# Kernel optimization log

Hardware: AMD Instinct MI355X
Metric: run time of the kernel (lower is better)

The kernel has to match this reference:

```python
import jax, jax.numpy as jnp
import numpy as np
import math

B, L, DIM, DEPTH, HEADS, DH, T, BUCKETS, MAXDIST = 256, 77, 768, 12, 12, 64, 1000, 32, 128
INNER = HEADS * DH            # 768
FF_IN = 4 * DIM               # 3072 (SwiGLU inner)
EPS = 1e-5


def rmsnorm(x, gamma):
    inv = jax.lax.rsqrt(jnp.sum(x * x, axis=-1, keepdims=True) + EPS)
    return x * inv * gamma * (DIM ** 0.5)


def rel_pos_bias(i, j, table):
    # table: [BUCKETS, HEADS] -> bias [HEADS, i, j]
    q_pos = jnp.arange(i)
    k_pos = jnp.arange(j)
    rel = k_pos[None, :] - q_pos[:, None]
    n = jnp.maximum(-rel, 0)
    max_exact = BUCKETS // 2
    is_small = n < max_exact
    nf = jnp.maximum(n, 1).astype(jnp.float32)
    val_large = max_exact + (jnp.log(nf / max_exact) / math.log(MAXDIST / max_exact) * (BUCKETS - max_exact)).astype(jnp.int32)
    val_large = jnp.minimum(val_large, BUCKETS - 1)
    bucket = jnp.where(is_small, n, val_large)
    return jnp.transpose(table[bucket], (2, 0, 1))  # h i j


def attention(x, mask, bias, gamma, Wq, Wkv, Wout, null_kv):
    b, n, _ = x.shape
    xn = rmsnorm(x, gamma)
    q = (xn @ Wq).reshape(b, n, HEADS, DH).transpose(0, 2, 1, 3)     # b h n d
    kv = xn @ Wkv                                                     # b n 2d (single head)
    k, v = kv[..., :DH], kv[..., DH:]
    nk = jnp.broadcast_to(null_kv[0], (b, 1, DH))
    nv = jnp.broadcast_to(null_kv[1], (b, 1, DH))
    k = jnp.concatenate([nk, k], axis=1)                              # b (n+1) d
    v = jnp.concatenate([nv, v], axis=1)
    sim = jnp.einsum('bhid,bjd->bhij', q * (DH ** -0.5), k) + bias[None]
    neg = -jnp.finfo(sim.dtype).max
    m = jnp.pad(mask, ((0, 0), (1, 0)), constant_values=True)         # null kv always visible
    sim = jnp.where(m[:, None, None, :], sim, neg)
    i, j = n, n + 1
    causal = jnp.arange(j)[None, :] > (jnp.arange(i)[:, None] + (j - i))
    sim = jnp.where(causal[None, None], neg, sim)
    attn = jax.nn.softmax(sim - jax.lax.stop_gradient(sim.max(axis=-1, keepdims=True)), axis=-1)
    out = jnp.einsum('bhij,bjd->bhid', attn, v)
    out = out.transpose(0, 2, 1, 3).reshape(b, n, INNER)
    return out @ Wout


def feedforward(x, gamma, W1, W2):
    h = rmsnorm(x, gamma) @ W1                                        # b n 2*FF_IN
    a, gate = h[..., :FF_IN], h[..., FF_IN:]
    return (a * jax.nn.silu(gate)) @ W2


def setup_inputs() -> dict:
    key = jax.random.key(0)
    ks = jax.random.split(key, 16)
    s = 0.02
    return {
        'image_embed': jax.random.normal(ks[0], (B, DIM), jnp.float32),
        'text_encodings': jax.random.normal(ks[1], (B, L, DIM), jnp.float32),
        'text_embed': jax.random.normal(ks[2], (B, DIM), jnp.float32),
        'time_emb_table': jax.random.normal(ks[3], (T, DIM), jnp.float32) * s,
        'learned_query': jax.random.normal(ks[4], (DIM,), jnp.float32),
        'rel_bias_table': jax.random.normal(ks[5], (BUCKETS, HEADS), jnp.float32) * s,
        'attn_gamma': jnp.ones((DEPTH, DIM), jnp.float32),
        'Wq': jax.random.normal(ks[6], (DEPTH, DIM, INNER), jnp.float32) * s,
        'Wkv': jax.random.normal(ks[7], (DEPTH, DIM, 2 * DH), jnp.float32) * s,
        'Wout': jax.random.normal(ks[8], (DEPTH, INNER, DIM), jnp.float32) * s,
        'null_kv': jax.random.normal(ks[9], (DEPTH, 2, DH), jnp.float32),
        'ff_gamma': jnp.ones((DEPTH, DIM), jnp.float32),
        'Wff1': jax.random.normal(ks[10], (DEPTH, DIM, 2 * FF_IN), jnp.float32) * s,
        'Wff2': jax.random.normal(ks[11], (DEPTH, FF_IN, DIM), jnp.float32) * s,
        'diffusion_timesteps': jax.random.randint(ks[12], (B,), 0, T),
        'mask': jnp.ones((B, L), dtype=bool),
    }


def reference(image_embed, text_encodings, text_embed, time_emb_table, learned_query,
              rel_bias_table, attn_gamma, Wq, Wkv, Wout, null_kv, ff_gamma, Wff1, Wff2,
              diffusion_timesteps, mask):
    b = image_embed.shape[0]
    # mask bookkeeping (matches torch forward); cond_drop_prob fixed at 1.0 -> keep all
    not_all = jnp.any(mask, axis=-1)
    m = jnp.concatenate([mask, not_all[:, None]], axis=1)
    m = jnp.pad(m, ((0, 0), (0, 2)), constant_values=True)            # [b, L+3]
    time_embed = time_emb_table[diffusion_timesteps][:, None, :]
    queries = jnp.broadcast_to(learned_query, (b, 1, DIM))
    tokens = jnp.concatenate([text_encodings, text_embed[:, None, :], time_embed, queries], axis=1)
    n = tokens.shape[1]
    bias = rel_pos_bias(n, n + 1, rel_bias_table)
    x = tokens
    for l in range(DEPTH):
        x = attention(x, m, bias, attn_gamma[l], Wq[l], Wkv[l], Wout[l], null_kv[l]) + x
        x = feedforward(x, ff_gamma[l], Wff1[l], Wff2[l]) + x
    return x[:, -1, :]
```

## Files before the change

### kernel.cpp

```cpp
#include <hip/hip_runtime.h>
#include <hip/hip_bf16.h>
#include <float.h>
#include <math.h>

#define NB 256
#define LTXT 77
#define DIM 768
#define DEPTH 12
#define HEADS 12
#define DH 64
#define NTOK 80
#define NKEY 81
#define NROWS (NB*NTOK)
#define FFH 3072
#define FF2C 6144
#define INNER 768
#define SROW 100

typedef __hip_bfloat16 bf16;
typedef __attribute__((ext_vector_type(8))) short short8;
typedef __attribute__((ext_vector_type(4))) float f32x4;

#define BARRIER() asm volatile("s_barrier" ::: "memory")
#define WAITV(n)  asm volatile("s_waitcnt vmcnt(" #n ")" ::: "memory")

__device__ __forceinline__ unsigned short f2bf(float f) {
    __hip_bfloat16 h = __float2bfloat16(f);
    return __builtin_bit_cast(unsigned short, h);
}

__global__ void build_tokens(const float* __restrict__ text_enc,
                             const float* __restrict__ text_emb,
                             const float* __restrict__ time_tab,
                             const float* __restrict__ lquery,
                             const int* __restrict__ tsteps,
                             float* __restrict__ x) {
    int idx = blockIdx.x * 256 + threadIdx.x;
    if (idx >= NROWS * DIM) return;
    int d = idx % DIM;
    int row = idx / DIM;
    int b = row / NTOK, p = row % NTOK;
    float v;
    if (p < LTXT)            v = text_enc[((size_t)b * LTXT + p) * DIM + d];
    else if (p == LTXT)      v = text_emb[(size_t)b * DIM + d];
    else if (p == LTXT + 1)  v = time_tab[(size_t)tsteps[b] * DIM + d];
    else                     v = lquery[d];
    x[idx] = v;
}

__global__ void build_biasR(const float* __restrict__ table, float* __restrict__ biasR) {
    int idx = blockIdx.x * 256 + threadIdx.x;
    if (idx >= HEADS * NTOK * 96) return;
    int kap = idx % 96;
    int i = (idx / 96) % NTOK;
    int h = idx / (96 * NTOK);
    float v;
    if ((kap < 80 && kap > i) || kap > 80) {
        v = -1e30f;
    } else {
        int j = (kap < 80) ? kap + 1 : 0;
        int rel = j - i;
        int n = rel < 0 ? -rel : 0;
        int bucket;
        if (n < 16) {
            bucket = n;
        } else {
            float val = logf((float)n / 16.0f) / logf(8.0f) * 16.0f;
            int vl = 16 + (int)val;
            bucket = vl < 31 ? vl : 31;
        }
        v = table[bucket * HEADS + h];
    }
    biasR[idx] = v;
}

__global__ __launch_bounds__(256) void convT(const float* __restrict__ W,
                                             bf16* __restrict__ WT,
                                             int K, int N) {
    __shared__ float t[32][33];
    int n0 = blockIdx.x * 32, k0 = blockIdx.y * 32;
    int tx = threadIdx.x & 31, ty = threadIdx.x >> 5;
    #pragma unroll
    for (int i = 0; i < 4; i++)
        t[ty + 8 * i][tx] = W[(size_t)(k0 + ty + 8 * i) * N + n0 + tx];
    __syncthreads();
    #pragma unroll
    for (int i = 0; i < 4; i++)
        WT[(size_t)(n0 + ty + 8 * i) * K + k0 + tx] = __float2bfloat16(t[tx][ty + 8 * i]);
}

__global__ __launch_bounds__(256) void rmsnorm_w(const float* __restrict__ x,
                                                 const float* __restrict__ gamma,
                                                 bf16* __restrict__ out) {
    int wave = blockIdx.x * 4 + (threadIdx.x >> 6);
    int lane = threadIdx.x & 63;
    float4 g0 = *(const float4*)&gamma[lane * 4];
    float4 g1 = *(const float4*)&gamma[lane * 4 + 256];
    float4 g2 = *(const float4*)&gamma[lane * 4 + 512];
    #pragma unroll 2
    for (int rr = 0; rr < 8; ++rr) {
        int row = wave * 8 + rr;
        const float* xr = x + (size_t)row * DIM + lane * 4;
        float4 v0 = *(const float4*)xr;
        float4 v1 = *(const float4*)(xr + 256);
        float4 v2 = *(const float4*)(xr + 512);
        float ss = v0.x*v0.x + v0.y*v0.y + v0.z*v0.z + v0.w*v0.w
                 + v1.x*v1.x + v1.y*v1.y + v1.z*v1.z + v1.w*v1.w
                 + v2.x*v2.x + v2.y*v2.y + v2.z*v2.z + v2.w*v2.w;
        #pragma unroll
        for (int o = 32; o > 0; o >>= 1) ss += __shfl_xor(ss, o);
        float inv = 27.712812921102035f / sqrtf(ss + 1e-5f);
        bf16* orow = out + (size_t)row * DIM + lane * 4;
        ushort4 w0 = { f2bf(v0.x*inv*g0.x), f2bf(v0.y*inv*g0.y), f2bf(v0.z*inv*g0.z), f2bf(v0.w*inv*g0.w) };
        ushort4 w1 = { f2bf(v1.x*inv*g1.x), f2bf(v1.y*inv*g1.y), f2bf(v1.z*inv*g1.z), f2bf(v1.w*inv*g1.w) };
        ushort4 w2 = { f2bf(v2.x*inv*g2.x), f2bf(v2.y*inv*g2.y), f2bf(v2.z*inv*g2.z), f2bf(v2.w*inv*g2.w) };
        *(ushort4*)(orow)       = w0;
        *(ushort4*)(orow + 256) = w1;
        *(ushort4*)(orow + 512) = w2;
    }
}


#define GSTAGE_N(nld, lds, base, b0, ld, kk0)                                  \
    _Pragma("unroll")                                                          \
    for (int r_ = 0; r_ < (nld); ++r_) {                                       \
        int idx_ = r_ * 256 + t;                                               \
        int row_ = idx_ >> 3, c_ = idx_ & 7;                                   \
        int cs_ = c_ ^ (row_ & 7);                                             \
        __builtin_amdgcn_global_load_lds(                                      \
            (const __attribute__((address_space(1))) unsigned int*)            \
                &base[(size_t)(b0 + row_) * ld + (kk0) + cs_ * 8],             \
            (__attribute__((address_space(3))) unsigned int*)&lds[idx_ * 8],   \
            16, 0, 0);                                                         \
    }

#define FRAG_READ(dst, lds, base_row, kk)                                      \
    _Pragma("unroll")                                                          \
    for (int q_ = 0; q_ < 4; ++q_) {                                           \
        int row_ = (base_row) + q_ * 16 + fr;                                  \
        int ch_ = ((((kk) << 2) + kb) ^ (row_ & 7));                           \
        dst[q_] = *(const short8*)&lds[row_ * 64 + ch_ * 8];                   \
    }

#define FRAG_READ2(dst, lds, base_row, kk)                                     \
    _Pragma("unroll")                                                          \
    for (int q_ = 0; q_ < 2; ++q_) {                                           \
        int row_ = (base_row) + q_ * 16 + fr;                                  \
        int ch_ = ((((kk) << 2) + kb) ^ (row_ & 7));                           \
        dst[q_] = *(const short8*)&lds[row_ * 64 + ch_ * 8];                   \
    }

template<int EPI>
__global__ __launch_bounds__(256, 2) void gemm_bt(const bf16* __restrict__ A,
                                                  const bf16* __restrict__ BT,
                                                  float* __restrict__ C,
                                                  int N, int K) {
    __shared__ __align__(16) short As[2 * 128 * 64];
    __shared__ __align__(16) short Bs[2 * 128 * 64];
    const int t = threadIdx.x;
    const int lane = t & 63;
    const int wid = t >> 6;
    const int wr = wid >> 1, wc = wid & 1;
    const int fr = lane & 15;
    const int kb = lane >> 4;
    const int row0 = blockIdx.y * 128, col0 = blockIdx.x * 128;

    f32x4 acc[4][4] = {};
    const int NKT = K >> 6;

    GSTAGE_N(4, As, A, row0, K, 0)
    GSTAGE_N(4, Bs, BT, col0, K, 0)

    for (int kt = 0; kt < NKT; ++kt) {
        const short* curA = As + (kt & 1) * (128 * 64);
        const short* curB = Bs + (kt & 1) * (128 * 64);
        if (kt + 1 < NKT) {
            short* nxtA = As + ((kt + 1) & 1) * (128 * 64);
            short* nxtB = Bs + ((kt + 1) & 1) * (128 * 64);
            int k0n = (kt + 1) << 6;
            GSTAGE_N(4, nxtA, A, row0, K, k0n)
            GSTAGE_N(4, nxtB, BT, col0, K, k0n)
            WAITV(8);
        } else {
            WAITV(0);
        }
        BARRIER();
        #pragma unroll
        for (int kk = 0; kk < 2; ++kk) {
            short8 af[4], bv[4];
            FRAG_READ(af, curA, wr * 64, kk)
            FRAG_READ(bv, curB, wc * 64, kk)
            __builtin_amdgcn_s_setprio(1);
            #pragma unroll
            for (int i = 0; i < 4; ++i)
                #pragma unroll
                for (int j = 0; j < 4; ++j)
                    acc[i][j] = __builtin_amdgcn_mfma_f32_16x16x32_bf16(af[i], bv[j], acc[i][j], 0, 0, 0);
            __builtin_amdgcn_s_setprio(0);
        }
        BARRIER();
    }

    #pragma unroll
    for (int i = 0; i < 4; ++i) {
        #pragma unroll
        for (int j = 0; j < 4; ++j) {
            int row = row0 + wr * 64 + i * 16 + kb * 4;
            int col = col0 + wc * 64 + j * 16 + fr;
            #pragma unroll
            for (int r = 0; r < 4; ++r) {
                size_t o = (size_t)(row + r) * N + col;
                if (EPI == 1)      C[o] += acc[i][j][r];
                else               ((bf16*)C)[o] = __float2bfloat16(acc[i][j][r]);
            }
        }
    }
}

__global__ __launch_bounds__(256, 2) void gemm_kv(const bf16* __restrict__ A,
                                                  const bf16* __restrict__ BT,
                                                  bf16* __restrict__ kout,
                                                  bf16* __restrict__ vT) {
    __shared__ __align__(16) short As[2 * 128 * 64];
    __shared__ __align__(16) short Bs[2 * 128 * 64];
    const int t = threadIdx.x;
    const int lane = t & 63;
    const int wid = t >> 6;
    const int wr = wid >> 1, wc = wid & 1;
    const int fr = lane & 15;
    const int kb = lane >> 4;
    const int row0 = blockIdx.y * 128;
    const int K = DIM;

    f32x4 acc[4][4] = {};
    const int NKT = DIM >> 6;

    GSTAGE_N(4, As, A, row0, K, 0)
    GSTAGE_N(4, Bs, BT, 0, K, 0)

    for (int kt = 0; kt < NKT; ++kt) {
        const short* curA = As + (kt & 1) * (128 * 64);
        const short* curB = Bs + (kt & 1) * (128 * 64);
        if (kt + 1 < NKT) {
            short* nxtA = As + ((kt + 1) & 1) * (128 * 64);
            short* nxtB = Bs + ((kt + 1) & 1) * (128 * 64);
            int k0n = (kt + 1) << 6;
            GSTAGE_N(4, nxtA, A, row0, K, k0n)
            GSTAGE_N(4, nxtB, BT, 0, K, k0n)
            WAITV(8);
        } else {
            WAITV(0);
        }
        BARRIER();
        #pragma unroll
        for (int kk = 0; kk < 2; ++kk) {
            short8 af[4], bv[4];
            FRAG_READ(af, curA, wr * 64, kk)
            FRAG_READ(bv, curB, wc * 64, kk)
            __builtin_amdgcn_s_setprio(1);
            #pragma unroll
            for (int i = 0; i < 4; ++i)
                #pragma unroll
                for (int j = 0; j < 4; ++j)
                    acc[i][j] = __builtin_amdgcn_mfma_f32_16x16x32_bf16(af[i], bv[j], acc[i][j], 0, 0, 0);
            __builtin_amdgcn_s_setprio(0);
        }
        BARRIER();
    }

    #pragma unroll
    for (int i = 0; i < 4; ++i) {
        #pragma unroll
        for (int j = 0; j < 4; ++j) {
            int row = row0 + wr * 64 + i * 16 + kb * 4;
            int col = wc * 64 + j * 16 + fr;
            #pragma unroll
            for (int r = 0; r < 4; ++r) {
                int rg = row + r;
                float v = acc[i][j][r];
                if (wc == 0) {
                    kout[(size_t)rg * 64 + col] = __float2bfloat16(v);
                } else {
                    int bb = rg / NTOK, ii = rg - bb * NTOK;
                    vT[((size_t)bb * 64 + (col - 64)) * NTOK + ii] = __float2bfloat16(v);
                }
            }
        }
    }
}

__global__ __launch_bounds__(256) void attn_mfma(const bf16* __restrict__ qb,
                                                 const bf16* __restrict__ kbuf,
                                                 const bf16* __restrict__ vT,
                                                 const float* __restrict__ nullkv,
                                                 const float* __restrict__ biasR,
                                                 bf16* __restrict__ attnb) {
    const int b = blockIdx.x / HEADS;
    const int h = blockIdx.x % HEADS;
    __shared__ __align__(16) short Ks[96 * 64];
    __shared__ __align__(16) short Vt[64 * 128];
    __shared__ __align__(16) float Sls[80 * SROW];
    char* Sb = (char*)Sls;
    const int t = threadIdx.x;
    const int lane = t & 63;
    const int wid = t >> 6;
    const int g = lane >> 4;
    const int fr = lane & 15;

    for (int c = t; c < 768; c += 256) {
        int row = c >> 3, ch = c & 7;
        short8 v;
        if (row < NTOK) {
            v = *(const short8*)&kbuf[((size_t)(b * NTOK + row)) * 64 + ch * 8];
        } else if (row == NTOK) {
            #pragma unroll
            for (int e = 0; e < 8; ++e) v[e] = (short)f2bf(nullkv[ch * 8 + e]);
        } else {
            v = short8{0,0,0,0,0,0,0,0};
        }
        *(short8*)((char*)Ks + row * 128 + ((ch ^ (row & 7)) << 4)) = v;
    }
    for (int c = t; c < 1024; c += 256) {
        int d = c >> 4, ch = c & 15;
        if (ch >= 12) continue;
        short8 v;
        if (ch < 10) {
            v = *(const short8*)&vT[((size_t)b * 64 + d) * NTOK + ch * 8];
        } else if (ch == 10) {
            v = short8{0,0,0,0,0,0,0,0};
            v[0] = (short)f2bf(nullkv[64 + d]);
        } else {
            v = short8{0,0,0,0,0,0,0,0};
        }
        *(short8*)((char*)Vt + d * 256 + ((ch ^ (d & 7)) << 4)) = v;
    }
    __syncthreads();

    const bf16* qbase = qb + ((size_t)(b * NTOK)) * INNER + h * DH;
    for (int s = 0; s < 8; ++s) {
        int tt = wid + 4 * s;
        if (tt >= 30) break;
        int m = tt / 6, n = tt - 6 * m;
        f32x4 acc = {};
        #pragma unroll
        for (int kk = 0; kk < 2; ++kk) {
            short8 a = *(const short8*)&qbase[(size_t)(m * 16 + fr) * INNER + kk * 32 + g * 8];
            int krow = n * 16 + fr;
            short8 kf = *(const short8*)((const char*)Ks + krow * 128 + ((((kk << 2) + g) ^ (krow & 7)) << 4));
            acc = __builtin_amdgcn_mfma_f32_16x16x32_bf16(a, kf, acc, 0, 0, 0);
        }
        int i0 = m * 16 + g * 4;
        int kap = n * 16 + fr;
        const float* bR = biasR + ((size_t)h * NTOK + i0) * 96 + kap;
        #pragma unroll
        for (int r = 0; r < 4; ++r)
            Sls[(i0 + r) * SROW + kap] = acc[r] * 0.125f + bR[r * 96];
    }
    __syncthreads();

    for (int rr = 0; rr < 20; ++rr) {
        int row = wid + 4 * rr;
        const float* Srow = Sls + row * SROW;
        float s0 = Srow[lane];
        float s1v = Srow[64 + (lane & 31)];
        float mx = fmaxf(s0, s1v);
        #pragma unroll
        for (int o = 32; o > 0; o >>= 1) mx = fmaxf(mx, __shfl_xor(mx, o));
        float e0 = __expf(s0 - mx);
        float e1 = (lane < 32) ? __expf(s1v - mx) : 0.0f;
        float sum = e0 + e1;
        #pragma unroll
        for (int o = 32; o > 0; o >>= 1) sum += __shfl_xor(sum, o);
        float inv = 1.0f / sum;
        *(unsigned short*)(Sb + row * (SROW * 4) + lane * 2) = f2bf(e0 * inv);
        if (lane < 32)
            *(unsigned short*)(Sb + row * (SROW * 4) + 128 + lane * 2) = f2bf(e1 * inv);
    }
    __syncthreads();

    for (int s = 0; s < 5; ++s) {
        int tt = wid + 4 * s;
        int m = tt >> 2, n = tt & 3;
        f32x4 acc = {};
        #pragma unroll
        for (int kc = 0; kc < 3; ++kc) {
            short8 p = *(const short8*)(Sb + (m * 16 + fr) * (SROW * 4) + kc * 64 + g * 16);
            int drow = n * 16 + fr;
            short8 vv = *(const short8*)((const char*)Vt + drow * 256 + ((((kc << 2) + g) ^ (drow & 7)) << 4));
            acc = __builtin_amdgcn_mfma_f32_16x16x32_bf16(p, vv, acc, 0, 0, 0);
        }
        int i0 = m * 16 + g * 4;
        int d = n * 16 + fr;
        #pragma unroll
        for (int r = 0; r < 4; ++r)
            attnb[((size_t)(b * NTOK) + i0 + r) * INNER + h * DH + d] = __float2bfloat16(acc[r]);
    }
}

__global__ __launch_bounds__(256, 2) void gemm_ff1(const bf16* __restrict__ A,
                                                   const bf16* __restrict__ W1T,
                                                   bf16* __restrict__ act) {
    __shared__ __align__(16) short As[2 * 128 * 64];
    __shared__ __align__(16) short Bs1[2 * 64 * 64];
    __shared__ __align__(16) short Bs2[2 * 64 * 64];
    const int t = threadIdx.x;
    const int lane = t & 63;
    const int wid = t >> 6;
    const int wr = wid >> 1, wc = wid & 1;
    const int fr = lane & 15;
    const int kb = lane >> 4;
    const int row0 = blockIdx.y * 128, col0 = blockIdx.x * 64;
    const int K = DIM;
    const bf16* B1 = W1T;
    const bf16* B2 = W1T + (size_t)FFH * DIM;

    f32x4 acc1[4][2] = {}, acc2[4][2] = {};
    const int NKT = DIM >> 6;

    GSTAGE_N(4, As, A, row0, K, 0)
    GSTAGE_N(2, Bs1, B1, col0, K, 0)
    GSTAGE_N(2, Bs2, B2, col0, K, 0)

    for (int kt = 0; kt < NKT; ++kt) {
        const short* curA  = As  + (kt & 1) * (128 * 64);
        const short* curB1 = Bs1 + (kt & 1) * (64 * 64);
        const short* curB2 = Bs2 + (kt & 1) * (64 * 64);
        if (kt + 1 < NKT) {
            short* nxtA  = As  + ((kt + 1) & 1) * (128 * 64);
            short* nxtB1 = Bs1 + ((kt + 1) & 1) * (64 * 64);
            short* nxtB2 = Bs2 + ((kt + 1) & 1) * (64 * 64);
            int k0n = (kt + 1) << 6;
            GSTAGE_N(4, nxtA, A, row0, K, k0n)
            GSTAGE_N(2, nxtB1, B1, col0, K, k0n)
            GSTAGE_N(2, nxtB2, B2, col0, K, k0n)
            WAITV(8);
        } else {
            WAITV(0);
        }
        BARRIER();
        #pragma unroll
        for (int kk = 0; kk < 2; ++kk) {
            short8 af[4], b1v[2], b2v[2];
            FRAG_READ(af, curA, wr * 64, kk)
            FRAG_READ2(b1v, curB1, wc * 32, kk)
            FRAG_READ2(b2v, curB2, wc * 32, kk)
            __builtin_amdgcn_s_setprio(1);
            #pragma unroll
            for (int i = 0; i < 4; ++i)
                #pragma unroll
                for (int j = 0; j < 2; ++j) {
                    acc1[i][j] = __builtin_amdgcn_mfma_f32_16x16x32_bf16(af[i], b1v[j], acc1[i][j], 0, 0, 0);
                    acc2[i][j] = __builtin_amdgcn_mfma_f32_16x16x32_bf16(af[i], b2v[j], acc2[i][j], 0, 0, 0);
                }
            __builtin_amdgcn_s_setprio(0);
        }
        BARRIER();
    }

    #pragma unroll
    for (int i = 0; i < 4; ++i) {
        #pragma unroll
        for (int j = 0; j < 2; ++j) {
            int row = row0 + wr * 64 + i * 16 + kb * 4;
            int col = col0 + wc * 32 + j * 16 + fr;
            #pragma unroll
            for (int r = 0; r < 4; ++r) {
                float a = acc1[i][j][r];
                float gt = acc2[i][j][r];
                float s = a * gt / (1.0f + __expf(-gt));
                act[(size_t)(row + r) * FFH + col] = __float2bfloat16(s);
            }
        }
    }
}

__global__ void extract(const float* __restrict__ x, float* __restrict__ out) {
    int idx = blockIdx.x * 256 + threadIdx.x;
    if (idx >= NB * DIM) return;
    int b = idx / DIM, d = idx % DIM;
    out[idx] = x[((size_t)(b * NTOK + NTOK - 1)) * DIM + d];
}

extern "C" void kernel_launch(void* const* d_in, const int* in_sizes, int n_in,
                              void* d_out, int out_size, void* d_ws, size_t ws_size,
                              hipStream_t stream) {
    (void)in_sizes; (void)n_in; (void)out_size; (void)ws_size;
    const float* text_enc = (const float*)d_in[1];
    const float* text_emb = (const float*)d_in[2];
    const float* time_tab = (const float*)d_in[3];
    const float* lquery   = (const float*)d_in[4];
    const float* rel_tab  = (const float*)d_in[5];
    const float* attn_g   = (const float*)d_in[6];
    const float* Wq       = (const float*)d_in[7];
    const float* Wkv      = (const float*)d_in[8];
    const float* Wout     = (const float*)d_in[9];
    const float* null_kv  = (const float*)d_in[10];
    const float* ff_g     = (const float*)d_in[11];
    const float* Wff1     = (const float*)d_in[12];
    const float* Wff2     = (const float*)d_in[13];
    const int*   tsteps   = (const int*)d_in[14];

    char* ws = (char*)d_ws;
    float* x     = (float*)(ws);
    bf16*  xn    = (bf16*)(ws + 62914560);
    bf16*  attnb = xn;
    char*  U     = ws + 94371840;
    bf16*  qb    = (bf16*)U;
    bf16*  kbuf  = (bf16*)(U + 31457280);
    bf16*  vT    = (bf16*)(U + 34078720);
    bf16*  act   = (bf16*)U;
    float* biasR = (float*)(ws + 220200960);
    bf16*  WqT   = (bf16*)(ws + 220569600);
    bf16*  WkvT  = (bf16*)(ws + 221749248);
    bf16*  WoutT = (bf16*)(ws + 221945856);
    bf16*  Wff1T = (bf16*)(ws + 223125504);
    bf16*  Wff2T = (bf16*)(ws + 232562688);

    build_tokens<<<(NROWS * DIM + 255) / 256, 256, 0, stream>>>(text_enc, text_emb, time_tab, lquery, tsteps, x);
    build_biasR<<<(HEADS * NTOK * 96 + 255) / 256, 256, 0, stream>>>(rel_tab, biasR);

    for (int l = 0; l < DEPTH; l++) {
        convT<<<dim3(INNER / 32, DIM / 32), 256, 0, stream>>>(Wq   + (size_t)l * DIM * INNER,  WqT,   DIM,   INNER);
        convT<<<dim3((2 * DH) / 32, DIM / 32), 256, 0, stream>>>(Wkv + (size_t)l * DIM * 2 * DH, WkvT, DIM, 2 * DH);
        convT<<<dim3(DIM / 32, INNER / 32), 256, 0, stream>>>(Wout + (size_t)l * INNER * DIM,  WoutT, INNER, DIM);
        convT<<<dim3(FF2C / 32, DIM / 32), 256, 0, stream>>>(Wff1 + (size_t)l * DIM * FF2C,    Wff1T, DIM,   FF2C);
        convT<<<dim3(DIM / 32, FFH / 32), 256, 0, stream>>>(Wff2  + (size_t)l * FFH * DIM,     Wff2T, FFH,   DIM);

        rmsnorm_w<<<NROWS / (8 * 4), 256, 0, stream>>>(x, attn_g + (size_t)l * DIM, xn);
        gemm_bt<2><<<dim3(INNER / 128, NROWS / 128), 256, 0, stream>>>(xn, WqT, (float*)qb, INNER, DIM);
        gemm_kv<<<dim3(1, NROWS / 128), 256, 0, stream>>>(xn, WkvT, kbuf, vT);
        attn_mfma<<<NB * HEADS, 256, 0, stream>>>(qb, kbuf, vT, null_kv + (size_t)l * 2 * DH, biasR, attnb);
        gemm_bt<1><<<dim3(DIM / 128, NROWS / 128), 256, 0, stream>>>(attnb, WoutT, x, DIM, INNER);

        rmsnorm_w<<<NROWS / (8 * 4), 256, 0, stream>>>(x, ff_g + (size_t)l * DIM, xn);
        gemm_ff1<<<dim3(FFH / 64, NROWS / 128), 256, 0, stream>>>(xn, Wff1T, act);
        gemm_bt<1><<<dim3(DIM / 128, NROWS / 128), 256, 0, stream>>>(act, Wff2T, x, DIM, FFH);
    }

    extract<<<(NB * DIM + 255) / 256, 256, 0, stream>>>(x, (float*)d_out);
}
```

Measured before the change: 7.894 ms.

## Switch GEMMs to 256x256 tiles with 8 waves and split A-tile prefetch

The 128-tile GEMM kernels are replaced with 256-row tile versions that use 512 threads (8 waves). Each wave computes 128 rows, handled as two halves. The next A tile is prefetched between the two half-compute phases, while the B tile is loaded ahead of them, so global loads overlap with MFMA work. The larger tiles raise data reuse per LDS byte and cut global traffic. In exchange, each block needs more LDS and more accumulator registers, and the N=768 GEMMs launch only 240 blocks, which may leave CUs idle.

```diff
diff --git a/kernel.cpp b/kernel.cpp
--- a/kernel.cpp
+++ b/kernel.cpp
@@ -134,6 +134,19 @@
             16, 0, 0);                                                         \
     }
 
+#define GSTAGE512(nld, lds, base, b0, ld, kk0)                                 \
+    _Pragma("unroll")                                                          \
+    for (int r_ = 0; r_ < (nld); ++r_) {                                       \
+        int idx_ = r_ * 512 + t;                                               \
+        int row_ = idx_ >> 3, c_ = idx_ & 7;                                   \
+        int cs_ = c_ ^ (row_ & 7);                                             \
+        __builtin_amdgcn_global_load_lds(                                      \
+            (const __attribute__((address_space(1))) unsigned int*)            \
+                &base[(size_t)(b0 + row_) * ld + (kk0) + cs_ * 8],             \
+            (__attribute__((address_space(3))) unsigned int*)&lds[idx_ * 8],   \
+            16, 0, 0);                                                         \
+    }
+
 #define FRAG_READ(dst, lds, base_row, kk)                                      \
     _Pragma("unroll")                                                          \
     for (int q_ = 0; q_ < 4; ++q_) {                                           \
@@ -142,76 +155,217 @@
         dst[q_] = *(const short8*)&lds[row_ * 64 + ch_ * 8];                   \
     }
 
-#define FRAG_READ2(dst, lds, base_row, kk)                                     \
-    _Pragma("unroll")                                                          \
-    for (int q_ = 0; q_ < 2; ++q_) {                                           \
-        int row_ = (base_row) + q_ * 16 + fr;                                  \
-        int ch_ = ((((kk) << 2) + kb) ^ (row_ & 7));                           \
-        dst[q_] = *(const short8*)&lds[row_ * 64 + ch_ * 8];                   \
-    }
+#define LDS_FRAG(lds, row_, kk)                                                \
+    (*(const short8*)&(lds)[(row_) * 64 + ((((kk) << 2) + kb) ^ ((row_) & 7)) * 8])
 
 template<int EPI>
-__global__ __launch_bounds__(256, 2) void gemm_bt(const bf16* __restrict__ A,
-                                                  const bf16* __restrict__ BT,
-                                                  float* __restrict__ C,
-                                                  int N, int K) {
-    __shared__ __align__(16) short As[2 * 128 * 64];
-    __shared__ __align__(16) short Bs[2 * 128 * 64];
+__global__ __launch_bounds__(512, 2) void gemm_bt256(const bf16* __restrict__ A,
+                                                     const bf16* __restrict__ BT,
+                                                     float* __restrict__ C,
+                                                     int N, int K) {
+    __shared__ __align__(16) short As[2 * 256 * 64];
+    __shared__ __align__(16) short Bs[2 * 256 * 64];
     const int t = threadIdx.x;
     const int lane = t & 63;
     const int wid = t >> 6;
-    const int wr = wid >> 1, wc = wid & 1;
+    const int wr = wid >> 2;
+    const int wn = wid & 3;
     const int fr = lane & 15;
     const int kb = lane >> 4;
-    const int row0 = blockIdx.y * 128, col0 = blockIdx.x * 128;
-
-    f32x4 acc[4][4] = {};
+    const int row0 = blockIdx.y * 256, col0 = blockIdx.x * 256;
+
+    f32x4 acc[8][4] = {};
     const int NKT = K >> 6;
 
-    GSTAGE_N(4, As, A, row0, K, 0)
-    GSTAGE_N(4, Bs, BT, col0, K, 0)
+    GSTAGE512(4, Bs, BT, col0, K, 0)
+    GSTAGE512(4, As, A, row0, K, 0)
 
     for (int kt = 0; kt < NKT; ++kt) {
-        const short* curA = As + (kt & 1) * (128 * 64);
-        const short* curB = Bs + (kt & 1) * (128 * 64);
+        const short* curA = As + (kt & 1) * (256 * 64);
+        const short* curB = Bs + (kt & 1) * (256 * 64);
+        short* nxtA = As + ((kt + 1) & 1) * (256 * 64);
+        short* nxtB = Bs + ((kt + 1) & 1) * (256 * 64);
+        const int k0n = (kt + 1) << 6;
+
+        short8 bv[4][2];
         if (kt + 1 < NKT) {
-            short* nxtA = As + ((kt + 1) & 1) * (128 * 64);
-            short* nxtB = Bs + ((kt + 1) & 1) * (128 * 64);
-            int k0n = (kt + 1) << 6;
-            GSTAGE_N(4, nxtA, A, row0, K, k0n)
-            GSTAGE_N(4, nxtB, BT, col0, K, k0n)
-            WAITV(8);
+            GSTAGE512(4, nxtB, BT, col0, K, k0n)
+            WAITV(4);
         } else {
             WAITV(0);
         }
         BARRIER();
-        #pragma unroll
-        for (int kk = 0; kk < 2; ++kk) {
-            short8 af[4], bv[4];
-            FRAG_READ(af, curA, wr * 64, kk)
-            FRAG_READ(bv, curB, wc * 64, kk)
+        {
+            #pragma unroll
+            for (int n = 0; n < 4; ++n)
+                #pragma unroll
+                for (int kk = 0; kk < 2; ++kk)
+                    bv[n][kk] = LDS_FRAG(curB, wn * 64 + n * 16 + fr, kk);
+            short8 af[4][2];
+            #pragma unroll
+            for (int m = 0; m < 4; ++m)
+                #pragma unroll
+                for (int kk = 0; kk < 2; ++kk)
+                    af[m][kk] = LDS_FRAG(curA, wr * 128 + m * 16 + fr, kk);
             __builtin_amdgcn_s_setprio(1);
             #pragma unroll
-            for (int i = 0; i < 4; ++i)
-                #pragma unroll
-                for (int j = 0; j < 4; ++j)
-                    acc[i][j] = __builtin_amdgcn_mfma_f32_16x16x32_bf16(af[i], bv[j], acc[i][j], 0, 0, 0);
+            for (int kk = 0; kk < 2; ++kk)
+                #pragma unroll
+                for (int m = 0; m < 4; ++m)
+                    #pragma unroll
+                    for (int n = 0; n < 4; ++n)
+                        acc[m][n] = __builtin_amdgcn_mfma_f32_16x16x32_bf16(af[m][kk], bv[n][kk], acc[m][n], 0, 0, 0);
             __builtin_amdgcn_s_setprio(0);
         }
         BARRIER();
+        if (kt + 1 < NKT) {
+            GSTAGE512(4, nxtA, A, row0, K, k0n)
+        }
+        BARRIER();
+        {
+            short8 af[4][2];
+            #pragma unroll
+            for (int m = 0; m < 4; ++m)
+                #pragma unroll
+                for (int kk = 0; kk < 2; ++kk)
+                    af[m][kk] = LDS_FRAG(curA, wr * 128 + (m + 4) * 16 + fr, kk);
+            __builtin_amdgcn_s_setprio(1);
+            #pragma unroll
+            for (int kk = 0; kk < 2; ++kk)
+                #pragma unroll
+                for (int m = 0; m < 4; ++m)
+                    #pragma unroll
+                    for (int n = 0; n < 4; ++n)
+                        acc[m + 4][n] = __builtin_amdgcn_mfma_f32_16x16x32_bf16(af[m][kk], bv[n][kk], acc[m + 4][n], 0, 0, 0);
+            __builtin_amdgcn_s_setprio(0);
+        }
+        BARRIER();
     }
 
     #pragma unroll
-    for (int i = 0; i < 4; ++i) {
-        #pragma unroll
-        for (int j = 0; j < 4; ++j) {
-            int row = row0 + wr * 64 + i * 16 + kb * 4;
-            int col = col0 + wc * 64 + j * 16 + fr;
+    for (int m = 0; m < 8; ++m) {
+        #pragma unroll
+        for (int n = 0; n < 4; ++n) {
+            int row = row0 + wr * 128 + m * 16 + kb * 4;
+            int col = col0 + wn * 64 + n * 16 + fr;
             #pragma unroll
             for (int r = 0; r < 4; ++r) {
                 size_t o = (size_t)(row + r) * N + col;
-                if (EPI == 1)      C[o] += acc[i][j][r];
-                else               ((bf16*)C)[o] = __float2bfloat16(acc[i][j][r]);
+                if (EPI == 1)      C[o] += acc[m][n][r];
+                else               ((bf16*)C)[o] = __float2bfloat16(acc[m][n][r]);
+            }
+        }
+    }
+}
+
+__global__ __launch_bounds__(512, 2) void gemm_ff1_256(const bf16* __restrict__ A,
+                                                       const bf16* __restrict__ W1T,
+                                                       bf16* __restrict__ act) {
+    __shared__ __align__(16) short As[2 * 256 * 64];
+    __shared__ __align__(16) short Bs1[2 * 128 * 64];
+    __shared__ __align__(16) short Bs2[2 * 128 * 64];
+    const int t = threadIdx.x;
+    const int lane = t & 63;
+    const int wid = t >> 6;
+    const int wr = wid >> 2;
+    const int wn = wid & 3;
+    const int fr = lane & 15;
+    const int kb = lane >> 4;
+    const int row0 = blockIdx.y * 256, col0 = blockIdx.x * 128;
+    const int K = DIM;
+    const bf16* B1 = W1T;
+    const bf16* B2 = W1T + (size_t)FFH * DIM;
+
+    f32x4 acc1[8][2] = {}, acc2[8][2] = {};
+    const int NKT = DIM >> 6;
+
+    GSTAGE512(2, Bs1, B1, col0, K, 0)
+    GSTAGE512(2, Bs2, B2, col0, K, 0)
+    GSTAGE512(4, As, A, row0, K, 0)
+
+    for (int kt = 0; kt < NKT; ++kt) {
+        const short* curA  = As  + (kt & 1) * (256 * 64);
+        const short* curB1 = Bs1 + (kt & 1) * (128 * 64);
+        const short* curB2 = Bs2 + (kt & 1) * (128 * 64);
+        short* nxtA  = As  + ((kt + 1) & 1) * (256 * 64);
+        short* nxtB1 = Bs1 + ((kt + 1) & 1) * (128 * 64);
+        short* nxtB2 = Bs2 + ((kt + 1) & 1) * (128 * 64);
+        const int k0n = (kt + 1) << 6;
+
+        short8 b1v[2][2], b2v[2][2];
+        if (kt + 1 < NKT) {
+            GSTAGE512(2, nxtB1, B1, col0, K, k0n)
+            GSTAGE512(2, nxtB2, B2, col0, K, k0n)
+            WAITV(4);
+        } else {
+            WAITV(0);
+        }
+        BARRIER();
+        {
+            #pragma unroll
+            for (int n = 0; n < 2; ++n)
+                #pragma unroll
+                for (int kk = 0; kk < 2; ++kk) {
+                    b1v[n][kk] = LDS_FRAG(curB1, wn * 32 + n * 16 + fr, kk);
+                    b2v[n][kk] = LDS_FRAG(curB2, wn * 32 + n * 16 + fr, kk);
+                }
+            short8 af[4][2];
+            #pragma unroll
+            for (int m = 0; m < 4; ++m)
+                #pragma unroll
+                for (int kk = 0; kk < 2; ++kk)
+                    af[m][kk] = LDS_FRAG(curA, wr * 128 + m * 16 + fr, kk);
+            __builtin_amdgcn_s_setprio(1);
+            #pragma unroll
+            for (int kk = 0; kk < 2; ++kk)
+                #pragma unroll
+                for (int m = 0; m < 4; ++m)
+                    #pragma unroll
+                    for (int n = 0; n < 2; ++n) {
+                        acc1[m][n] = __builtin_amdgcn_mfma_f32_16x16x32_bf16(af[m][kk], b1v[n][kk], acc1[m][n], 0, 0, 0);
+                        acc2[m][n] = __builtin_amdgcn_mfma_f32_16x16x32_bf16(af[m][kk], b2v[n][kk], acc2[m][n], 0, 0, 0);
+                    }
+            __builtin_amdgcn_s_setprio(0);
+        }
+        BARRIER();
+        if (kt + 1 < NKT) {
+            GSTAGE512(4, nxtA, A, row0, K, k0n)
+        }
+        BARRIER();
+        {
+            short8 af[4][2];
+            #pragma unroll
+            for (int m = 0; m < 4; ++m)
+                #pragma unroll
+                for (int kk = 0; kk < 2; ++kk)
+                    af[m][kk] = LDS_FRAG(curA, wr * 128 + (m + 4) * 16 + fr, kk);
+            __builtin_amdgcn_s_setprio(1);
+            #pragma unroll
+            for (int kk = 0; kk < 2; ++kk)
+                #pragma unroll
+                for (int m = 0; m < 4; ++m)
+                    #pragma unroll
+                    for (int n = 0; n < 2; ++n) {
+                        acc1[m + 4][n] = __builtin_amdgcn_mfma_f32_16x16x32_bf16(af[m][kk], b1v[n][kk], acc1[m + 4][n], 0, 0, 0);
+                        acc2[m + 4][n] = __builtin_amdgcn_mfma_f32_16x16x32_bf16(af[m][kk], b2v[n][kk], acc2[m + 4][n], 0, 0, 0);
+                    }
+            __builtin_amdgcn_s_setprio(0);
+        }
+        BARRIER();
+    }
+
+    #pragma unroll
+    for (int m = 0; m < 8; ++m) {
+        #pragma unroll
+        for (int n = 0; n < 2; ++n) {
+            int row = row0 + wr * 128 + m * 16 + kb * 4;
+            int col = col0 + wn * 32 + n * 16 + fr;
+            #pragma unroll
+            for (int r = 0; r < 4; ++r) {
+                float a = acc1[m][n][r];
+                float gt = acc2[m][n][r];
+                float s = a * gt / (1.0f + __expf(-gt));
+                act[(size_t)(row + r) * FFH + col] = __float2bfloat16(s);
             }
         }
     }
@@ -394,83 +548,6 @@
         #pragma unroll
         for (int r = 0; r < 4; ++r)
             attnb[((size_t)(b * NTOK) + i0 + r) * INNER + h * DH + d] = __float2bfloat16(acc[r]);
-    }
-}
-
-__global__ __launch_bounds__(256, 2) void gemm_ff1(const bf16* __restrict__ A,
-                                                   const bf16* __restrict__ W1T,
-                                                   bf16* __restrict__ act) {
-    __shared__ __align__(16) short As[2 * 128 * 64];
-    __shared__ __align__(16) short Bs1[2 * 64 * 64];
-    __shared__ __align__(16) short Bs2[2 * 64 * 64];
-    const int t = threadIdx.x;
-    const int lane = t & 63;
-    const int wid = t >> 6;
-    const int wr = wid >> 1, wc = wid & 1;
-    const int fr = lane & 15;
-    const int kb = lane >> 4;
-    const int row0 = blockIdx.y * 128, col0 = blockIdx.x * 64;
-    const int K = DIM;
-    const bf16* B1 = W1T;
-    const bf16* B2 = W1T + (size_t)FFH * DIM;
-
-    f32x4 acc1[4][2] = {}, acc2[4][2] = {};
-    const int NKT = DIM >> 6;
-
-    GSTAGE_N(4, As, A, row0, K, 0)
-    GSTAGE_N(2, Bs1, B1, col0, K, 0)
-    GSTAGE_N(2, Bs2, B2, col0, K, 0)
-
-    for (int kt = 0; kt < NKT; ++kt) {
-        const short* curA  = As  + (kt & 1) * (128 * 64);
-        const short* curB1 = Bs1 + (kt & 1) * (64 * 64);
-        const short* curB2 = Bs2 + (kt & 1) * (64 * 64);
-        if (kt + 1 < NKT) {
-            short* nxtA  = As  + ((kt + 1) & 1) * (128 * 64);
-            short* nxtB1 = Bs1 + ((kt + 1) & 1) * (64 * 64);
-            short* nxtB2 = Bs2 + ((kt + 1) & 1) * (64 * 64);
-            int k0n = (kt + 1) << 6;
-            GSTAGE_N(4, nxtA, A, row0, K, k0n)
-            GSTAGE_N(2, nxtB1, B1, col0, K, k0n)
-            GSTAGE_N(2, nxtB2, B2, col0, K, k0n)
-            WAITV(8);
-        } else {
-            WAITV(0);
-        }
-        BARRIER();
-        #pragma unroll
-        for (int kk = 0; kk < 2; ++kk) {
-            short8 af[4], b1v[2], b2v[2];
-            FRAG_READ(af, curA, wr * 64, kk)
-            FRAG_READ2(b1v, curB1, wc * 32, kk)
-            FRAG_READ2(b2v, curB2, wc * 32, kk)
-            __builtin_amdgcn_s_setprio(1);
-            #pragma unroll
-            for (int i = 0; i < 4; ++i)
-                #pragma unroll
-                for (int j = 0; j < 2; ++j) {
-                    acc1[i][j] = __builtin_amdgcn_mfma_f32_16x16x32_bf16(af[i], b1v[j], acc1[i][j], 0, 0, 0);
-                    acc2[i][j] = __builtin_amdgcn_mfma_f32_16x16x32_bf16(af[i], b2v[j], acc2[i][j], 0, 0, 0);
-                }
-            __builtin_amdgcn_s_setprio(0);
-        }
-        BARRIER();
-    }
-
-    #pragma unroll
-    for (int i = 0; i < 4; ++i) {
-        #pragma unroll
-        for (int j = 0; j < 2; ++j) {
-            int row = row0 + wr * 64 + i * 16 + kb * 4;
-            int col = col0 + wc * 32 + j * 16 + fr;
-            #pragma unroll
-            for (int r = 0; r < 4; ++r) {
-                float a = acc1[i][j][r];
-                float gt = acc2[i][j][r];
-                float s = a * gt / (1.0f + __expf(-gt));
-                act[(size_t)(row + r) * FFH + col] = __float2bfloat16(s);
-            }
-        }
     }
 }
 
@@ -527,14 +604,14 @@
         convT<<<dim3(DIM / 32, FFH / 32), 256, 0, stream>>>(Wff2  + (size_t)l * FFH * DIM,     Wff2T, FFH,   DIM);
 
         rmsnorm_w<<<NROWS / (8 * 4), 256, 0, stream>>>(x, attn_g + (size_t)l * DIM, xn);
-        gemm_bt<2><<<dim3(INNER / 128, NROWS / 128), 256, 0, stream>>>(xn, WqT, (float*)qb, INNER, DIM);
+        gemm_bt256<2><<<dim3(INNER / 256, NROWS / 256), 512, 0, stream>>>(xn, WqT, (float*)qb, INNER, DIM);
         gemm_kv<<<dim3(1, NROWS / 128), 256, 0, stream>>>(xn, WkvT, kbuf, vT);
         attn_mfma<<<NB * HEADS, 256, 0, stream>>>(qb, kbuf, vT, null_kv + (size_t)l * 2 * DH, biasR, attnb);
-        gemm_bt<1><<<dim3(DIM / 128, NROWS / 128), 256, 0, stream>>>(attnb, WoutT, x, DIM, INNER);
+        gemm_bt256<1><<<dim3(DIM / 256, NROWS / 256), 512, 0, stream>>>(attnb, WoutT, x, DIM, INNER);
 
         rmsnorm_w<<<NROWS / (8 * 4), 256, 0, stream>>>(x, ff_g + (size_t)l * DIM, xn);
-        gemm_ff1<<<dim3(FFH / 64, NROWS / 128), 256, 0, stream>>>(xn, Wff1T, act);
-        gemm_bt<1><<<dim3(DIM / 128, NROWS / 128), 256, 0, stream>>>(act, Wff2T, x, DIM, FFH);
+        gemm_ff1_256<<<dim3(FFH / 128, NROWS / 256), 512, 0, stream>>>(xn, Wff1T, act);
+        gemm_bt256<1><<<dim3(DIM / 256, NROWS / 256), 512, 0, stream>>>(act, Wff2T, x, DIM, FFH);
     }
 
     extract<<<(NB * DIM + 255) / 256, 256, 0, stream>>>(x, (float*)d_out);
```

Result: no change. 8.004 ms (+1.4%).

## Switch GEMMs to 32x32x16 MFMA and fuse Q and KV projections

Applied to the files above, without the earlier changes.

Replaces the 16x16x32 bf16 MFMA tiles in all GEMM kernels with 32x32x16 MFMA tiles. Each wave now holds 2x2 32x32 accumulators, which roughly halves the LDS fragment reads per unit of work and uses the higher-throughput instruction shape. The Q projection and the KV projection are also merged into one GEMM over a concatenated transposed weight, with a column-dependent epilogue, removing one launch and a second read of the normalized activations. The epilogue stores become strided across rows in a different pattern, which may change write coalescing.

```diff
diff --git a/kernel.cpp b/kernel.cpp
--- a/kernel.cpp
+++ b/kernel.cpp
@@ -20,6 +20,7 @@
 typedef __hip_bfloat16 bf16;
 typedef __attribute__((ext_vector_type(8))) short short8;
 typedef __attribute__((ext_vector_type(4))) float f32x4;
+typedef __attribute__((ext_vector_type(16))) float f32x16;
 
 #define BARRIER() asm volatile("s_barrier" ::: "memory")
 #define WAITV(n)  asm volatile("s_waitcnt vmcnt(" #n ")" ::: "memory")
@@ -134,38 +135,26 @@
             16, 0, 0);                                                         \
     }
 
-#define FRAG_READ(dst, lds, base_row, kk)                                      \
-    _Pragma("unroll")                                                          \
-    for (int q_ = 0; q_ < 4; ++q_) {                                           \
-        int row_ = (base_row) + q_ * 16 + fr;                                  \
-        int ch_ = ((((kk) << 2) + kb) ^ (row_ & 7));                           \
-        dst[q_] = *(const short8*)&lds[row_ * 64 + ch_ * 8];                   \
-    }
-
-#define FRAG_READ2(dst, lds, base_row, kk)                                     \
-    _Pragma("unroll")                                                          \
-    for (int q_ = 0; q_ < 2; ++q_) {                                           \
-        int row_ = (base_row) + q_ * 16 + fr;                                  \
-        int ch_ = ((((kk) << 2) + kb) ^ (row_ & 7));                           \
-        dst[q_] = *(const short8*)&lds[row_ * 64 + ch_ * 8];                   \
-    }
+#define FRAG32(lds, base_row, mm, kk)                                          \
+    (*(const short8*)&(lds)[((base_row) + (mm) * 32 + fr32) * 64 +             \
+        ((((kk) * 2 + hk) ^ (((base_row) + (mm) * 32 + fr32) & 7)) * 8)])
 
 template<int EPI>
-__global__ __launch_bounds__(256, 2) void gemm_bt(const bf16* __restrict__ A,
-                                                  const bf16* __restrict__ BT,
-                                                  float* __restrict__ C,
-                                                  int N, int K) {
+__global__ __launch_bounds__(256, 2) void gemm_bt32(const bf16* __restrict__ A,
+                                                    const bf16* __restrict__ BT,
+                                                    float* __restrict__ C,
+                                                    int N, int K) {
     __shared__ __align__(16) short As[2 * 128 * 64];
     __shared__ __align__(16) short Bs[2 * 128 * 64];
     const int t = threadIdx.x;
     const int lane = t & 63;
     const int wid = t >> 6;
     const int wr = wid >> 1, wc = wid & 1;
-    const int fr = lane & 15;
-    const int kb = lane >> 4;
+    const int fr32 = lane & 31;
+    const int hk = lane >> 5;
     const int row0 = blockIdx.y * 128, col0 = blockIdx.x * 128;
 
-    f32x4 acc[4][4] = {};
+    f32x16 acc[2][2] = {};
     const int NKT = K >> 6;
 
     GSTAGE_N(4, As, A, row0, K, 0)
@@ -185,58 +174,69 @@
             WAITV(0);
         }
         BARRIER();
-        #pragma unroll
-        for (int kk = 0; kk < 2; ++kk) {
-            short8 af[4], bv[4];
-            FRAG_READ(af, curA, wr * 64, kk)
-            FRAG_READ(bv, curB, wc * 64, kk)
+        {
+            short8 af[2][4], bv[2][4];
+            #pragma unroll
+            for (int m = 0; m < 2; ++m)
+                #pragma unroll
+                for (int kk = 0; kk < 4; ++kk)
+                    af[m][kk] = FRAG32(curA, wr * 64, m, kk);
+            #pragma unroll
+            for (int n = 0; n < 2; ++n)
+                #pragma unroll
+                for (int kk = 0; kk < 4; ++kk)
+                    bv[n][kk] = FRAG32(curB, wc * 64, n, kk);
             __builtin_amdgcn_s_setprio(1);
             #pragma unroll
-            for (int i = 0; i < 4; ++i)
-                #pragma unroll
-                for (int j = 0; j < 4; ++j)
-                    acc[i][j] = __builtin_amdgcn_mfma_f32_16x16x32_bf16(af[i], bv[j], acc[i][j], 0, 0, 0);
+            for (int kk = 0; kk < 4; ++kk)
+                #pragma unroll
+                for (int m = 0; m < 2; ++m)
+                    #pragma unroll
+                    for (int n = 0; n < 2; ++n)
+                        acc[m][n] = __builtin_amdgcn_mfma_f32_32x32x16_bf16(af[m][kk], bv[n][kk], acc[m][n], 0, 0, 0);
             __builtin_amdgcn_s_setprio(0);
         }
         BARRIER();
     }
 
     #pragma unroll
-    for (int i = 0; i < 4; ++i) {
-        #pragma unroll
-        for (int j = 0; j < 4; ++j) {
-            int row = row0 + wr * 64 + i * 16 + kb * 4;
-            int col = col0 + wc * 64 + j * 16 + fr;
-            #pragma unroll
-            for (int r = 0; r < 4; ++r) {
-                size_t o = (size_t)(row + r) * N + col;
-                if (EPI == 1)      C[o] += acc[i][j][r];
-                else               ((bf16*)C)[o] = __float2bfloat16(acc[i][j][r]);
+    for (int m = 0; m < 2; ++m) {
+        #pragma unroll
+        for (int n = 0; n < 2; ++n) {
+            int brow = row0 + wr * 64 + m * 32 + 4 * hk;
+            int col = col0 + wc * 64 + n * 32 + fr32;
+            #pragma unroll
+            for (int r = 0; r < 16; ++r) {
+                int row = brow + (r & 3) + 8 * (r >> 2);
+                size_t o = (size_t)row * N + col;
+                if (EPI == 1)      C[o] += acc[m][n][r];
+                else               ((bf16*)C)[o] = __float2bfloat16(acc[m][n][r]);
             }
         }
     }
 }
 
-__global__ __launch_bounds__(256, 2) void gemm_kv(const bf16* __restrict__ A,
-                                                  const bf16* __restrict__ BT,
-                                                  bf16* __restrict__ kout,
-                                                  bf16* __restrict__ vT) {
+__global__ __launch_bounds__(256, 2) void gemm_qkv32(const bf16* __restrict__ A,
+                                                     const bf16* __restrict__ BT,
+                                                     bf16* __restrict__ qb,
+                                                     bf16* __restrict__ kout,
+                                                     bf16* __restrict__ vT) {
     __shared__ __align__(16) short As[2 * 128 * 64];
     __shared__ __align__(16) short Bs[2 * 128 * 64];
     const int t = threadIdx.x;
     const int lane = t & 63;
     const int wid = t >> 6;
     const int wr = wid >> 1, wc = wid & 1;
-    const int fr = lane & 15;
-    const int kb = lane >> 4;
-    const int row0 = blockIdx.y * 128;
+    const int fr32 = lane & 31;
+    const int hk = lane >> 5;
+    const int row0 = blockIdx.y * 128, col0 = blockIdx.x * 128;
     const int K = DIM;
 
-    f32x4 acc[4][4] = {};
+    f32x16 acc[2][2] = {};
     const int NKT = DIM >> 6;
 
     GSTAGE_N(4, As, A, row0, K, 0)
-    GSTAGE_N(4, Bs, BT, 0, K, 0)
+    GSTAGE_N(4, Bs, BT, col0, K, 0)
 
     for (int kt = 0; kt < NKT; ++kt) {
         const short* curA = As + (kt & 1) * (128 * 64);
@@ -246,45 +246,151 @@
             short* nxtB = Bs + ((kt + 1) & 1) * (128 * 64);
             int k0n = (kt + 1) << 6;
             GSTAGE_N(4, nxtA, A, row0, K, k0n)
-            GSTAGE_N(4, nxtB, BT, 0, K, k0n)
+            GSTAGE_N(4, nxtB, BT, col0, K, k0n)
             WAITV(8);
         } else {
             WAITV(0);
         }
         BARRIER();
-        #pragma unroll
-        for (int kk = 0; kk < 2; ++kk) {
-            short8 af[4], bv[4];
-            FRAG_READ(af, curA, wr * 64, kk)
-            FRAG_READ(bv, curB, wc * 64, kk)
+        {
+            short8 af[2][4], bv[2][4];
+            #pragma unroll
+            for (int m = 0; m < 2; ++m)
+                #pragma unroll
+                for (int kk = 0; kk < 4; ++kk)
+                    af[m][kk] = FRAG32(curA, wr * 64, m, kk);
+            #pragma unroll
+            for (int n = 0; n < 2; ++n)
+                #pragma unroll
+                for (int kk = 0; kk < 4; ++kk)
+                    bv[n][kk] = FRAG32(curB, wc * 64, n, kk);
             __builtin_amdgcn_s_setprio(1);
             #pragma unroll
-            for (int i = 0; i < 4; ++i)
-                #pragma unroll
-                for (int j = 0; j < 4; ++j)
-                    acc[i][j] = __builtin_amdgcn_mfma_f32_16x16x32_bf16(af[i], bv[j], acc[i][j], 0, 0, 0);
+            for (int kk = 0; kk < 4; ++kk)
+                #pragma unroll
+                for (int m = 0; m < 2; ++m)
+                    #pragma unroll
+                    for (int n = 0; n < 2; ++n)
+                        acc[m][n] = __builtin_amdgcn_mfma_f32_32x32x16_bf16(af[m][kk], bv[n][kk], acc[m][n], 0, 0, 0);
             __builtin_amdgcn_s_setprio(0);
         }
         BARRIER();
     }
 
-    #pragma unroll
-    for (int i = 0; i < 4; ++i) {
-        #pragma unroll
-        for (int j = 0; j < 4; ++j) {
-            int row = row0 + wr * 64 + i * 16 + kb * 4;
-            int col = wc * 64 + j * 16 + fr;
-            #pragma unroll
-            for (int r = 0; r < 4; ++r) {
-                int rg = row + r;
-                float v = acc[i][j][r];
-                if (wc == 0) {
-                    kout[(size_t)rg * 64 + col] = __float2bfloat16(v);
-                } else {
-                    int bb = rg / NTOK, ii = rg - bb * NTOK;
-                    vT[((size_t)bb * 64 + (col - 64)) * NTOK + ii] = __float2bfloat16(v);
+    if (col0 < 768) {
+        #pragma unroll
+        for (int m = 0; m < 2; ++m) {
+            #pragma unroll
+            for (int n = 0; n < 2; ++n) {
+                int brow = row0 + wr * 64 + m * 32 + 4 * hk;
+                int col = col0 + wc * 64 + n * 32 + fr32;
+                #pragma unroll
+                for (int r = 0; r < 16; ++r) {
+                    int row = brow + (r & 3) + 8 * (r >> 2);
+                    qb[(size_t)row * INNER + col] = __float2bfloat16(acc[m][n][r]);
                 }
             }
+        }
+    } else {
+        #pragma unroll
+        for (int m = 0; m < 2; ++m) {
+            #pragma unroll
+            for (int n = 0; n < 2; ++n) {
+                int brow = row0 + wr * 64 + m * 32 + 4 * hk;
+                int c = wc * 64 + n * 32 + fr32;
+                #pragma unroll
+                for (int r = 0; r < 16; ++r) {
+                    int row = brow + (r & 3) + 8 * (r >> 2);
+                    float v = acc[m][n][r];
+                    if (c < 64) {
+                        kout[(size_t)row * 64 + c] = __float2bfloat16(v);
+                    } else {
+                        int bb = row / NTOK, ii = row - bb * NTOK;
+                        vT[((size_t)bb * 64 + (c - 64)) * NTOK + ii] = __float2bfloat16(v);
+                    }
+                }
+            }
+        }
+    }
+}
+
+__global__ __launch_bounds__(256, 2) void gemm_ff1_32(const bf16* __restrict__ A,
+                                                      const bf16* __restrict__ W1T,
+                                                      bf16* __restrict__ act) {
+    __shared__ __align__(16) short As[2 * 128 * 64];
+    __shared__ __align__(16) short Bs1[2 * 64 * 64];
+    __shared__ __align__(16) short Bs2[2 * 64 * 64];
+    const int t = threadIdx.x;
+    const int lane = t & 63;
+    const int wid = t >> 6;
+    const int wr = wid >> 1, wc = wid & 1;
+    const int fr32 = lane & 31;
+    const int hk = lane >> 5;
+    const int row0 = blockIdx.y * 128, col0 = blockIdx.x * 64;
+    const int K = DIM;
+    const bf16* B1 = W1T;
+    const bf16* B2 = W1T + (size_t)FFH * DIM;
+
+    f32x16 acc1[2] = {}, acc2[2] = {};
+    const int NKT = DIM >> 6;
+
+    GSTAGE_N(4, As, A, row0, K, 0)
+    GSTAGE_N(2, Bs1, B1, col0, K, 0)
+    GSTAGE_N(2, Bs2, B2, col0, K, 0)
+
+    for (int kt = 0; kt < NKT; ++kt) {
+        const short* curA  = As  + (kt & 1) * (128 * 64);
+        const short* curB1 = Bs1 + (kt & 1) * (64 * 64);
+        const short* curB2 = Bs2 + (kt & 1) * (64 * 64);
+        if (kt + 1 < NKT) {
+            short* nxtA  = As  + ((kt + 1) & 1) * (128 * 64);
+            short* nxtB1 = Bs1 + ((kt + 1) & 1) * (64 * 64);
+            short* nxtB2 = Bs2 + ((kt + 1) & 1) * (64 * 64);
+            int k0n = (kt + 1) << 6;
+            GSTAGE_N(4, nxtA, A, row0, K, k0n)
+            GSTAGE_N(2, nxtB1, B1, col0, K, k0n)
+            GSTAGE_N(2, nxtB2, B2, col0, K, k0n)
+            WAITV(8);
+        } else {
+            WAITV(0);
+        }
+        BARRIER();
+        {
+            short8 af[2][4], b1v[4], b2v[4];
+            #pragma unroll
+            for (int m = 0; m < 2; ++m)
+                #pragma unroll
+                for (int kk = 0; kk < 4; ++kk)
+                    af[m][kk] = FRAG32(curA, wr * 64, m, kk);
+            #pragma unroll
+            for (int kk = 0; kk < 4; ++kk) {
+                b1v[kk] = FRAG32(curB1, wc * 32, 0, kk);
+                b2v[kk] = FRAG32(curB2, wc * 32, 0, kk);
+            }
+            __builtin_amdgcn_s_setprio(1);
+            #pragma unroll
+            for (int kk = 0; kk < 4; ++kk)
+                #pragma unroll
+                for (int m = 0; m < 2; ++m) {
+                    acc1[m] = __builtin_amdgcn_mfma_f32_32x32x16_bf16(af[m][kk], b1v[kk], acc1[m], 0, 0, 0);
+                    acc2[m] = __builtin_amdgcn_mfma_f32_32x32x16_bf16(af[m][kk], b2v[kk], acc2[m], 0, 0, 0);
+                }
+            __builtin_amdgcn_s_setprio(0);
+        }
+        BARRIER();
+    }
+
+    #pragma unroll
+    for (int m = 0; m < 2; ++m) {
+        int brow = row0 + wr * 64 + m * 32 + 4 * hk;
+        int col = col0 + wc * 32 + fr32;
+        #pragma unroll
+        for (int r = 0; r < 16; ++r) {
+            int row = brow + (r & 3) + 8 * (r >> 2);
+            float a = acc1[m][r];
+            float gt = acc2[m][r];
+            float s = a * gt / (1.0f + __expf(-gt));
+            act[(size_t)row * FFH + col] = __float2bfloat16(s);
         }
     }
 }
@@ -394,83 +500,6 @@
         #pragma unroll
         for (int r = 0; r < 4; ++r)
             attnb[((size_t)(b * NTOK) + i0 + r) * INNER + h * DH + d] = __float2bfloat16(acc[r]);
-    }
-}
-
-__global__ __launch_bounds__(256, 2) void gemm_ff1(const bf16* __restrict__ A,
-                                                   const bf16* __restrict__ W1T,
-                                                   bf16* __restrict__ act) {
-    __shared__ __align__(16) short As[2 * 128 * 64];
-    __shared__ __align__(16) short Bs1[2 * 64 * 64];
-    __shared__ __align__(16) short Bs2[2 * 64 * 64];
-    const int t = threadIdx.x;
-    const int lane = t & 63;
-    const int wid = t >> 6;
-    const int wr = wid >> 1, wc = wid & 1;
-    const int fr = lane & 15;
-    const int kb = lane >> 4;
-    const int row0 = blockIdx.y * 128, col0 = blockIdx.x * 64;
-    const int K = DIM;
-    const bf16* B1 = W1T;
-    const bf16* B2 = W1T + (size_t)FFH * DIM;
-
-    f32x4 acc1[4][2] = {}, acc2[4][2] = {};
-    const int NKT = DIM >> 6;
-
-    GSTAGE_N(4, As, A, row0, K, 0)
-    GSTAGE_N(2, Bs1, B1, col0, K, 0)
-    GSTAGE_N(2, Bs2, B2, col0, K, 0)
-
-    for (int kt = 0; kt < NKT; ++kt) {
-        const short* curA  = As  + (kt & 1) * (128 * 64);
-        const short* curB1 = Bs1 + (kt & 1) * (64 * 64);
-        const short* curB2 = Bs2 + (kt & 1) * (64 * 64);
-        if (kt + 1 < NKT) {
-            short* nxtA  = As  + ((kt + 1) & 1) * (128 * 64);
-            short* nxtB1 = Bs1 + ((kt + 1) & 1) * (64 * 64);
-            short* nxtB2 = Bs2 + ((kt + 1) & 1) * (64 * 64);
-            int k0n = (kt + 1) << 6;
-            GSTAGE_N(4, nxtA, A, row0, K, k0n)
-            GSTAGE_N(2, nxtB1, B1, col0, K, k0n)
-            GSTAGE_N(2, nxtB2, B2, col0, K, k0n)
-            WAITV(8);
-        } else {
-            WAITV(0);
-        }
-        BARRIER();
-        #pragma unroll
-        for (int kk = 0; kk < 2; ++kk) {
-            short8 af[4], b1v[2], b2v[2];
-            FRAG_READ(af, curA, wr * 64, kk)
-            FRAG_READ2(b1v, curB1, wc * 32, kk)
-            FRAG_READ2(b2v, curB2, wc * 32, kk)
-            __builtin_amdgcn_s_setprio(1);
-            #pragma unroll
-            for (int i = 0; i < 4; ++i)
-                #pragma unroll
-                for (int j = 0; j < 2; ++j) {
-                    acc1[i][j] = __builtin_amdgcn_mfma_f32_16x16x32_bf16(af[i], b1v[j], acc1[i][j], 0, 0, 0);
-                    acc2[i][j] = __builtin_amdgcn_mfma_f32_16x16x32_bf16(af[i], b2v[j], acc2[i][j], 0, 0, 0);
-                }
-            __builtin_amdgcn_s_setprio(0);
-        }
-        BARRIER();
-    }
-
-    #pragma unroll
-    for (int i = 0; i < 4; ++i) {
-        #pragma unroll
-        for (int j = 0; j < 2; ++j) {
-            int row = row0 + wr * 64 + i * 16 + kb * 4;
-            int col = col0 + wc * 32 + j * 16 + fr;
-            #pragma unroll
-            for (int r = 0; r < 4; ++r) {
-                float a = acc1[i][j][r];
-                float gt = acc2[i][j][r];
-                float s = a * gt / (1.0f + __expf(-gt));
-                act[(size_t)(row + r) * FFH + col] = __float2bfloat16(s);
-            }
-        }
     }
 }
 
@@ -510,8 +539,7 @@
     bf16*  vT    = (bf16*)(U + 34078720);
     bf16*  act   = (bf16*)U;
     float* biasR = (float*)(ws + 220200960);
-    bf16*  WqT   = (bf16*)(ws + 220569600);
-    bf16*  WkvT  = (bf16*)(ws + 221749248);
+    bf16*  WqkvT = (bf16*)(ws + 220569600);
     bf16*  WoutT = (bf16*)(ws + 221945856);
     bf16*  Wff1T = (bf16*)(ws + 223125504);
     bf16*  Wff2T = (bf16*)(ws + 232562688);
@@ -520,21 +548,20 @@
     build_biasR<<<(HEADS * NTOK * 96 + 255) / 256, 256, 0, stream>>>(rel_tab, biasR);
 
     for (int l = 0; l < DEPTH; l++) {
-        convT<<<dim3(INNER / 32, DIM / 32), 256, 0, stream>>>(Wq   + (size_t)l * DIM * INNER,  WqT,   DIM,   INNER);
-        convT<<<dim3((2 * DH) / 32, DIM / 32), 256, 0, stream>>>(Wkv + (size_t)l * DIM * 2 * DH, WkvT, DIM, 2 * DH);
+        convT<<<dim3(INNER / 32, DIM / 32), 256, 0, stream>>>(Wq   + (size_t)l * DIM * INNER,  WqkvT,               DIM, INNER);
+        convT<<<dim3((2 * DH) / 32, DIM / 32), 256, 0, stream>>>(Wkv + (size_t)l * DIM * 2 * DH, WqkvT + 768 * DIM, DIM, 2 * DH);
         convT<<<dim3(DIM / 32, INNER / 32), 256, 0, stream>>>(Wout + (size_t)l * INNER * DIM,  WoutT, INNER, DIM);
         convT<<<dim3(FF2C / 32, DIM / 32), 256, 0, stream>>>(Wff1 + (size_t)l * DIM * FF2C,    Wff1T, DIM,   FF2C);
         convT<<<dim3(DIM / 32, FFH / 32), 256, 0, stream>>>(Wff2  + (size_t)l * FFH * DIM,     Wff2T, FFH,   DIM);
 
         rmsnorm_w<<<NROWS / (8 * 4), 256, 0, stream>>>(x, attn_g + (size_t)l * DIM, xn);
-        gemm_bt<2><<<dim3(INNER / 128, NROWS / 128), 256, 0, stream>>>(xn, WqT, (float*)qb, INNER, DIM);
-        gemm_kv<<<dim3(1, NROWS / 128), 256, 0, stream>>>(xn, WkvT, kbuf, vT);
+        gemm_qkv32<<<dim3(896 / 128, NROWS / 128), 256, 0, stream>>>(xn, WqkvT, qb, kbuf, vT);
         attn_mfma<<<NB * HEADS, 256, 0, stream>>>(qb, kbuf, vT, null_kv + (size_t)l * 2 * DH, biasR, attnb);
-        gemm_bt<1><<<dim3(DIM / 128, NROWS / 128), 256, 0, stream>>>(attnb, WoutT, x, DIM, INNER);
+        gemm_bt32<1><<<dim3(DIM / 128, NROWS / 128), 256, 0, stream>>>(attnb, WoutT, x, DIM, INNER);
 
         rmsnorm_w<<<NROWS / (8 * 4), 256, 0, stream>>>(x, ff_g + (size_t)l * DIM, xn);
-        gemm_ff1<<<dim3(FFH / 64, NROWS / 128), 256, 0, stream>>>(xn, Wff1T, act);
-        gemm_bt<1><<<dim3(DIM / 128, NROWS / 128), 256, 0, stream>>>(act, Wff2T, x, DIM, FFH);
+        gemm_ff1_32<<<dim3(FFH / 64, NROWS / 128), 256, 0, stream>>>(xn, Wff1T, act);
+        gemm_bt32<1><<<dim3(DIM / 128, NROWS / 128), 256, 0, stream>>>(act, Wff2T, x, DIM, FFH);
     }
 
     extract<<<(NB * DIM + 255) / 256, 256, 0, stream>>>(x, (float*)d_out);
```

New measurement: 8.346 ms. 1.06x slower.
